# Optimization experiments

Measured on AMD Instinct MI355X. Metric: run time of the kernel, lower is better.

Reference implementation:

```python
import jax, jax.numpy as jnp
import numpy as np
import math

N_EMBED = 1024
N_HEAD = 16
BLOCK_SIZE = 2048

def setup_inputs() -> dict:
    key = jax.random.key(0)
    k1, k2, k3, k4, k5 = jax.random.split(key, 5)
    s = 0.02
    x = jax.random.normal(k1, (2, 2048, N_EMBED), dtype=jnp.float32)
    W_qkv = jax.random.normal(k2, (N_EMBED, 3 * N_EMBED), dtype=jnp.float32) * s
    b_qkv = jax.random.normal(k3, (3 * N_EMBED,), dtype=jnp.float32) * s
    W_out = jax.random.normal(k4, (N_EMBED, N_EMBED), dtype=jnp.float32) * s
    b_out = jax.random.normal(k5, (N_EMBED,), dtype=jnp.float32) * s
    return {"x": x, "W_qkv": W_qkv, "b_qkv": b_qkv, "W_out": W_out, "b_out": b_out}

def reference(x, W_qkv, b_qkv, W_out, b_out):
    b, s, d = x.shape
    hd = d // N_HEAD  # head dim
    qkv = x @ W_qkv + b_qkv                       # [b, s, 3d]
    q, k, v = jnp.split(qkv, 3, axis=-1)
    # [b, h, s, hd]
    q = q.reshape(b, s, N_HEAD, hd).transpose(0, 2, 1, 3)
    k = k.reshape(b, s, N_HEAD, hd).transpose(0, 2, 1, 3)
    v = v.reshape(b, s, N_HEAD, hd).transpose(0, 2, 1, 3)
    scale = 1.0 / math.sqrt(hd)
    sims = jnp.einsum('bhqd,bhkd->bhqk', q, k) * scale  # [b, h, s, s]
    causal = jnp.tril(jnp.ones((s, s), dtype=bool))
    sims = jnp.where(causal[None, None], sims, -jnp.inf)
    probs = jax.nn.softmax(sims, axis=-1)
    attn = jnp.einsum('bhqk,bhkd->bhqd', probs, v)       # [b, h, s, hd]
    attn = attn.transpose(0, 2, 1, 3).reshape(b, s, d)
    return attn @ W_out + b_out
```

## Files before the change

### kernel.cpp

```cpp
#include <hip/hip_runtime.h>
#include <hip/hip_bf16.h>

typedef __attribute__((ext_vector_type(8))) short short8;
typedef __attribute__((ext_vector_type(4))) short short4v;
typedef __attribute__((ext_vector_type(4))) float f32x4;
typedef __attribute__((ext_vector_type(16))) float f32x16;
typedef __attribute__((ext_vector_type(4))) unsigned int u32x4;
typedef unsigned short u16;

__device__ __forceinline__ u16 f2bf(float f) {
  __hip_bfloat16 h = __float2bfloat16(f);
  return __builtin_bit_cast(unsigned short, h);
}

__device__ __forceinline__ unsigned pack2(float lo, float hi) {
  return (unsigned)f2bf(lo) | ((unsigned)f2bf(hi) << 16);
}

__device__ __forceinline__ void gload16(const u16* g, u16* l) {
  __builtin_amdgcn_global_load_lds(
      (const __attribute__((address_space(1))) unsigned int*)g,
      (__attribute__((address_space(3))) unsigned int*)l, 16, 0, 0);
}

__global__ void prep_kernel(const float* __restrict__ x,
                            const float* __restrict__ Wqkv,
                            const float* __restrict__ Wout,
                            u16* __restrict__ Xb,
                            u16* __restrict__ WqkvT,
                            u16* __restrict__ WoutT) {
  __shared__ float tile[32][33];
  const int b = blockIdx.x, tid = threadIdx.x;
  if (b < 4096) {
    const int i = (b * 256 + tid) * 4;
    float4 f = *(const float4*)(x + i);
    uint2 pk;
    pk.x = pack2(f.x, f.y);
    pk.y = pack2(f.z, f.w);
    *(uint2*)(Xb + i) = pk;
    return;
  }
  const float* in;
  u16* out;
  int N, bx, by;
  if (b < 7168) {
    in = Wqkv; out = WqkvT; N = 3072;
    const int bb = b - 4096;
    bx = bb % 96; by = bb / 96;
  } else {
    in = Wout; out = WoutT; N = 1024;
    const int bb = b - 7168;
    bx = bb % 32; by = bb / 32;
  }
  const int n0 = bx * 32, k0 = by * 32;
  const int tx = tid & 31, ty = tid >> 5;
#pragma unroll
  for (int r = 0; r < 4; ++r) {
    const int k = ty + r * 8;
    tile[k][tx] = in[(size_t)(k0 + k) * N + n0 + tx];
  }
  __syncthreads();
#pragma unroll
  for (int r = 0; r < 4; ++r) {
    const int n = ty + r * 8;
    out[(size_t)(n0 + n) * 1024 + k0 + tx] = f2bf(tile[tx][n]);
  }
}

template <int EPI, int BN, int WPE>
__global__ __launch_bounds__(256, WPE) void gemm_kernel(const u16* __restrict__ A,
                                                        const u16* __restrict__ Bt,
                                                        const float* __restrict__ bias,
                                                        void* __restrict__ outp) {
  __shared__ u16 Al[128 * 64];
  __shared__ u16 Bl[BN * 64];
  constexpr int NF = BN / 32;
  const int tid = threadIdx.x;
  const int lane = tid & 63, wid = tid >> 6;
  const int l15 = lane & 15, lg = lane >> 4;
  const int wm = wid >> 1, wn = wid & 1;
  const int m0 = blockIdx.y * 128, n0 = blockIdx.x * BN;

  f32x4 acc[4][NF] = {};

  for (int k0 = 0; k0 < 1024; k0 += 64) {
    __syncthreads();
#pragma unroll
    for (int i = 0; i < 4; ++i) {
      const int p = i * 4096 + tid * 16;
      const int row = p >> 7;
      const int lslot = ((p >> 4) & 7) ^ (row & 7);
      gload16(A + (size_t)(m0 + row) * 1024 + k0 + lslot * 8, Al + i * 2048 + wid * 512);
    }
#pragma unroll
    for (int i = 0; i < NF; ++i) {
      const int p = i * 4096 + tid * 16;
      const int row = p >> 7;
      const int lslot = ((p >> 4) & 7) ^ (row & 7);
      gload16(Bt + (size_t)(n0 + row) * 1024 + k0 + lslot * 8, Bl + i * 2048 + wid * 512);
    }
    __syncthreads();
#pragma unroll
    for (int ks = 0; ks < 2; ++ks) {
      short8 af[4], bfr[NF];
#pragma unroll
      for (int m = 0; m < 4; ++m) {
        const int row = wm * 64 + m * 16 + l15;
        af[m] = *(const short8*)((const char*)Al + row * 128 + (((ks * 4 + lg) ^ (row & 7)) << 4));
      }
#pragma unroll
      for (int n = 0; n < NF; ++n) {
        const int row = wn * (BN / 2) + n * 16 + l15;
        bfr[n] = *(const short8*)((const char*)Bl + row * 128 + (((ks * 4 + lg) ^ (row & 7)) << 4));
      }
#pragma unroll
      for (int m = 0; m < 4; ++m)
#pragma unroll
        for (int n = 0; n < NF; ++n)
          acc[m][n] = __builtin_amdgcn_mfma_f32_16x16x32_bf16(af[m], bfr[n], acc[m][n], 0, 0, 0);
    }
  }

  if (EPI == 0) {
    u16* qkv = (u16*)outp;
#pragma unroll
    for (int m = 0; m < 4; ++m)
#pragma unroll
      for (int n = 0; n < NF; ++n) {
        const int gcol = n0 + wn * (BN / 2) + n * 16 + l15;
        const int which = gcol >> 10, dd = gcol & 1023;
        const int h = dd >> 6, hd = dd & 63;
        const float bb = bias[gcol];
        const int grow0 = m0 + wm * 64 + m * 16 + lg * 4;
        const int b = grow0 >> 11, s0 = grow0 & 2047;
        if (which == 2) {
          const int bsub = (s0 >> 2) & 3;
          const int bper = (bsub == 1) ? 2 : (bsub == 2) ? 1 : bsub;
          const int s0p = (s0 & ~15) | (bper << 2);
          short4v pk;
#pragma unroll
          for (int j = 0; j < 4; ++j) pk[j] = (short)f2bf(acc[m][n][j] + bb);
          *(short4v*)(qkv + (size_t)2 * 4194304 + ((size_t)(b * 16 + h) * 64 + hd) * 2048 + s0p) = pk;
        } else {
          const float sc = (which == 0) ? 0.18033688011112042f : 1.0f;
#pragma unroll
          for (int j = 0; j < 4; ++j) {
            float v = (acc[m][n][j] + bb) * sc;
            qkv[(size_t)which * 4194304 + ((size_t)(b * 16 + h) * 2048 + s0 + j) * 64 + hd] = f2bf(v);
          }
        }
      }
  } else {
    float* O = (float*)outp;
#pragma unroll
    for (int m = 0; m < 4; ++m)
#pragma unroll
      for (int n = 0; n < NF; ++n) {
        const int gcol = n0 + wn * (BN / 2) + n * 16 + l15;
        const float bb = bias[gcol];
#pragma unroll
        for (int j = 0; j < 4; ++j) {
          const int grow = m0 + wm * 64 + m * 16 + lg * 4 + j;
          O[(size_t)grow * 1024 + gcol] = acc[m][n][j] + bb;
        }
      }
  }
}

__global__ __launch_bounds__(512, 4) void attn_kernel(const u16* __restrict__ Q,
                                                      const u16* __restrict__ K,
                                                      const u16* __restrict__ VT,
                                                      u16* __restrict__ Aout) {
  const int d = blockIdx.x;
  const int xcd = d & 7, slot = d >> 3;
  const int bh = xcd + 8 * (slot >> 4);
  const int p = slot & 15;
  const int tid = threadIdx.x, lane = tid & 63, wid = tid >> 6;
  const int l31 = lane & 31, h = lane >> 5;
  const int tl = wid >> 2, qs = (wid >> 1) & 1, kp = wid & 1;

  __shared__ __align__(16) char smem[36864];
  u16(*Kl)[4096] = (u16(*)[4096])smem;
  u16(*Vl)[4096] = (u16(*)[4096])(smem + 16384);

  const u16* Qb = Q + (size_t)bh * 2048 * 64;
  const u16* Kb = K + (size_t)bh * 2048 * 64;
  const u16* Vb = VT + (size_t)bh * 64 * 2048;

  const int tile = tl ? p : (31 - p);
  const int q0 = tile * 64 + qs * 32;
  const int R = 32 - p;

  short8 qf[4];
#pragma unroll
  for (int ks = 0; ks < 4; ++ks)
    qf[ks] = *(const short8*)(Qb + (size_t)(q0 + l31) * 64 + ks * 16 + h * 8);

  short8 ones;
#pragma unroll
  for (int j = 0; j < 8; ++j) ones[j] = (short)0x3F80;

  f32x16 acc[2] = {};
  f32x16 acc_l = {};

  const int srow = tid >> 3;
  const int ssc = ((tid & 7) ^ (srow & 7)) * 8;
  auto stage = [&](int buf, size_t kb) {
    gload16(Kb + (kb + srow) * 64 + ssc, &Kl[buf][wid * 512]);
    gload16(Vb + (size_t)srow * 2048 + kb + ssc, &Vl[buf][wid * 512]);
  };

  stage(0, 0);
  __syncthreads();

  for (int t = 0; t < R; ++t) {
    const int cur = t & 1;
    if (t + 1 < R) stage(cur ^ 1, (size_t)(t + 1) * 64);

    const int kvbase = t * 64 + kp * 32;
    if (kvbase <= q0 + 31) {
      short8 kf[4], vf[2][2];
      const int krow = kp * 32 + l31;
#pragma unroll
      for (int ks = 0; ks < 4; ++ks)
        kf[ks] = *(const short8*)((const char*)&Kl[cur][0] + krow * 128 +
                                  (((ks * 2 + h) ^ (krow & 7)) << 4));
#pragma unroll
      for (int n = 0; n < 2; ++n)
#pragma unroll
        for (int ks = 0; ks < 2; ++ks) {
          const int row = n * 32 + l31;
          vf[n][ks] = *(const short8*)((const char*)&Vl[cur][0] + row * 128 +
                                       (((kp * 4 + ks * 2 + h) ^ (row & 7)) << 4));
        }

      f32x16 sa = {};
      __builtin_amdgcn_s_setprio(1);
#pragma unroll
      for (int ks = 0; ks < 4; ++ks)
        sa = __builtin_amdgcn_mfma_f32_32x32x16_bf16(kf[ks], qf[ks], sa, 0, 0, 0);
      __builtin_amdgcn_s_setprio(0);

      if (kvbase == q0) {
#pragma unroll
        for (int r = 0; r < 16; ++r) {
          const int kvr = (r & 3) + 8 * (r >> 2) + 4 * h;
          if (kvr > l31) sa[r] = -1e30f;
        }
      }
#pragma unroll
      for (int r = 0; r < 16; ++r) sa[r] = exp2f(sa[r]);
      unsigned c[8];
#pragma unroll
      for (int i = 0; i < 8; ++i) c[i] = pack2(sa[2 * i], sa[2 * i + 1]);
      const short8 pk0 = __builtin_bit_cast(short8, (u32x4){c[0], c[1], c[2], c[3]});
      const short8 pk1 = __builtin_bit_cast(short8, (u32x4){c[4], c[5], c[6], c[7]});
      __builtin_amdgcn_s_setprio(1);
      acc_l = __builtin_amdgcn_mfma_f32_32x32x16_bf16(ones, pk0, acc_l, 0, 0, 0);
      acc_l = __builtin_amdgcn_mfma_f32_32x32x16_bf16(ones, pk1, acc_l, 0, 0, 0);
#pragma unroll
      for (int n = 0; n < 2; ++n) {
        acc[n] = __builtin_amdgcn_mfma_f32_32x32x16_bf16(vf[n][0], pk0, acc[n], 0, 0, 0);
        acc[n] = __builtin_amdgcn_mfma_f32_32x32x16_bf16(vf[n][1], pk1, acc[n], 0, 0, 0);
      }
      __builtin_amdgcn_s_setprio(0);
    }
    __syncthreads();
  }

  float* pp = (float*)smem + (((tl << 1) | qs) * 64 + lane) * 36;
  if (kp == 1) {
    pp[0] = acc_l[0];
#pragma unroll
    for (int n = 0; n < 2; ++n)
#pragma unroll
      for (int r = 0; r < 16; ++r) pp[2 + n * 16 + r] = acc[n][r];
  }
  __syncthreads();
  if (kp == 0) {
    const int b = bh >> 4, hh = bh & 15;
    const float inv = 1.0f / (acc_l[0] + pp[0]);
    u16* rowp = Aout + (size_t)(b * 2048 + q0 + l31) * 1024 + hh * 64;
#pragma unroll
    for (int n = 0; n < 2; ++n)
#pragma unroll
      for (int r = 0; r < 16; r += 2) {
        const int hd = n * 32 + (r & 3) + 8 * (r >> 2) + 4 * h;
        const float v0 = (acc[n][r] + pp[2 + n * 16 + r]) * inv;
        const float v1 = (acc[n][r + 1] + pp[2 + n * 16 + r + 1]) * inv;
        *(unsigned*)(rowp + hd) = pack2(v0, v1);
      }
  }
}

extern "C" void kernel_launch(void* const* d_in, const int* in_sizes, int n_in,
                              void* d_out, int out_size, void* d_ws, size_t ws_size,
                              hipStream_t stream) {
  const float* x = (const float*)d_in[0];
  const float* Wqkv = (const float*)d_in[1];
  const float* bqkv = (const float*)d_in[2];
  const float* Wout = (const float*)d_in[3];
  const float* bout = (const float*)d_in[4];

  char* ws = (char*)d_ws;
  u16* Xb = (u16*)(ws + 0);
  u16* WqkvT = (u16*)(ws + 8388608);
  u16* WoutT = (u16*)(ws + 14680064);
  u16* QKV = (u16*)(ws + 16777216);
  u16* Attn = Xb;

  prep_kernel<<<8192, 256, 0, stream>>>(x, Wqkv, Wout, Xb, WqkvT, WoutT);
  gemm_kernel<0, 128, 3><<<dim3(24, 32), 256, 0, stream>>>(Xb, WqkvT, bqkv, QKV);
  attn_kernel<<<512, 512, 0, stream>>>(QKV, QKV + 4194304, QKV + 8388608, Attn);
  gemm_kernel<1, 64, 2><<<dim3(16, 32), 256, 0, stream>>>(Attn, WoutT, bout, d_out);
}
```

Baseline: 97.75 us.

## Fuse x fp32-to-bf16 conversion into QKV GEMM load; retile output GEMM

The separate conversion pass that turned x into bf16 in the prep kernel is removed. The QKV GEMM now reads fp32 x straight from global memory, packs it to bf16 in registers, and stores it into swizzled LDS. This saves a full write and re-read of the bf16 activation copy and shrinks the prep launch. The output projection GEMM moves to 64x64 tiles with more blocks and higher occupancy. The cost is that the QKV GEMM now issues synchronous fp32 loads with twice the bytes instead of async global-to-LDS copies, and these are re-read for each of the 24 column blocks.

```diff
diff --git a/kernel.cpp b/kernel.cpp
--- a/kernel.cpp
+++ b/kernel.cpp
@@ -23,33 +23,21 @@
       (__attribute__((address_space(3))) unsigned int*)l, 16, 0, 0);
 }
 
-__global__ void prep_kernel(const float* __restrict__ x,
-                            const float* __restrict__ Wqkv,
+__global__ void prep_kernel(const float* __restrict__ Wqkv,
                             const float* __restrict__ Wout,
-                            u16* __restrict__ Xb,
                             u16* __restrict__ WqkvT,
                             u16* __restrict__ WoutT) {
   __shared__ float tile[32][33];
   const int b = blockIdx.x, tid = threadIdx.x;
-  if (b < 4096) {
-    const int i = (b * 256 + tid) * 4;
-    float4 f = *(const float4*)(x + i);
-    uint2 pk;
-    pk.x = pack2(f.x, f.y);
-    pk.y = pack2(f.z, f.w);
-    *(uint2*)(Xb + i) = pk;
-    return;
-  }
   const float* in;
   u16* out;
   int N, bx, by;
-  if (b < 7168) {
+  if (b < 3072) {
     in = Wqkv; out = WqkvT; N = 3072;
-    const int bb = b - 4096;
-    bx = bb % 96; by = bb / 96;
+    bx = b % 96; by = b / 96;
   } else {
     in = Wout; out = WoutT; N = 1024;
-    const int bb = b - 7168;
+    const int bb = b - 3072;
     bx = bb % 32; by = bb / 32;
   }
   const int n0 = bx * 32, k0 = by * 32;
@@ -67,45 +55,62 @@
   }
 }
 
-template <int EPI, int BN, int WPE>
-__global__ __launch_bounds__(256, WPE) void gemm_kernel(const u16* __restrict__ A,
+template <int EPI, int BM, int BN, int WPE>
+__global__ __launch_bounds__(256, WPE) void gemm_kernel(const void* __restrict__ Ap,
                                                         const u16* __restrict__ Bt,
                                                         const float* __restrict__ bias,
                                                         void* __restrict__ outp) {
-  __shared__ u16 Al[128 * 64];
+  constexpr int MF = BM / 32;
+  constexpr int NF = BN / 32;
+  __shared__ u16 Al[BM * 64];
   __shared__ u16 Bl[BN * 64];
-  constexpr int NF = BN / 32;
   const int tid = threadIdx.x;
   const int lane = tid & 63, wid = tid >> 6;
   const int l15 = lane & 15, lg = lane >> 4;
   const int wm = wid >> 1, wn = wid & 1;
-  const int m0 = blockIdx.y * 128, n0 = blockIdx.x * BN;
-
-  f32x4 acc[4][NF] = {};
+  const int m0 = blockIdx.y * BM, n0 = blockIdx.x * BN;
+
+  f32x4 acc[MF][NF] = {};
 
   for (int k0 = 0; k0 < 1024; k0 += 64) {
     __syncthreads();
 #pragma unroll
-    for (int i = 0; i < 4; ++i) {
-      const int p = i * 4096 + tid * 16;
-      const int row = p >> 7;
-      const int lslot = ((p >> 4) & 7) ^ (row & 7);
-      gload16(A + (size_t)(m0 + row) * 1024 + k0 + lslot * 8, Al + i * 2048 + wid * 512);
-    }
-#pragma unroll
     for (int i = 0; i < NF; ++i) {
-      const int p = i * 4096 + tid * 16;
-      const int row = p >> 7;
-      const int lslot = ((p >> 4) & 7) ^ (row & 7);
+      const int row = i * 32 + (tid >> 3);
+      const int lslot = (tid & 7) ^ (row & 7);
       gload16(Bt + (size_t)(n0 + row) * 1024 + k0 + lslot * 8, Bl + i * 2048 + wid * 512);
     }
+    if (EPI == 0) {
+      const float* X = (const float*)Ap;
+#pragma unroll
+      for (int i = 0; i < MF; ++i) {
+        const int row = i * 32 + (tid >> 3);
+        const int slot = tid & 7;
+        const int lslot = slot ^ (row & 7);
+        const float* src = X + (size_t)(m0 + row) * 1024 + k0 + lslot * 8;
+        const float4 a = *(const float4*)src;
+        const float4 b = *(const float4*)(src + 4);
+        u32x4 w;
+        w[0] = pack2(a.x, a.y); w[1] = pack2(a.z, a.w);
+        w[2] = pack2(b.x, b.y); w[3] = pack2(b.z, b.w);
+        *(u32x4*)(Al + row * 64 + slot * 8) = w;
+      }
+    } else {
+      const u16* A = (const u16*)Ap;
+#pragma unroll
+      for (int i = 0; i < MF; ++i) {
+        const int row = i * 32 + (tid >> 3);
+        const int lslot = (tid & 7) ^ (row & 7);
+        gload16(A + (size_t)(m0 + row) * 1024 + k0 + lslot * 8, Al + i * 2048 + wid * 512);
+      }
+    }
     __syncthreads();
 #pragma unroll
     for (int ks = 0; ks < 2; ++ks) {
-      short8 af[4], bfr[NF];
-#pragma unroll
-      for (int m = 0; m < 4; ++m) {
-        const int row = wm * 64 + m * 16 + l15;
+      short8 af[MF], bfr[NF];
+#pragma unroll
+      for (int m = 0; m < MF; ++m) {
+        const int row = wm * (BM / 2) + m * 16 + l15;
         af[m] = *(const short8*)((const char*)Al + row * 128 + (((ks * 4 + lg) ^ (row & 7)) << 4));
       }
 #pragma unroll
@@ -114,7 +119,7 @@
         bfr[n] = *(const short8*)((const char*)Bl + row * 128 + (((ks * 4 + lg) ^ (row & 7)) << 4));
       }
 #pragma unroll
-      for (int m = 0; m < 4; ++m)
+      for (int m = 0; m < MF; ++m)
 #pragma unroll
         for (int n = 0; n < NF; ++n)
           acc[m][n] = __builtin_amdgcn_mfma_f32_16x16x32_bf16(af[m], bfr[n], acc[m][n], 0, 0, 0);
@@ -124,14 +129,14 @@
   if (EPI == 0) {
     u16* qkv = (u16*)outp;
 #pragma unroll
-    for (int m = 0; m < 4; ++m)
+    for (int m = 0; m < MF; ++m)
 #pragma unroll
       for (int n = 0; n < NF; ++n) {
         const int gcol = n0 + wn * (BN / 2) + n * 16 + l15;
         const int which = gcol >> 10, dd = gcol & 1023;
         const int h = dd >> 6, hd = dd & 63;
         const float bb = bias[gcol];
-        const int grow0 = m0 + wm * 64 + m * 16 + lg * 4;
+        const int grow0 = m0 + wm * (BM / 2) + m * 16 + lg * 4;
         const int b = grow0 >> 11, s0 = grow0 & 2047;
         if (which == 2) {
           const int bsub = (s0 >> 2) & 3;
@@ -153,14 +158,14 @@
   } else {
     float* O = (float*)outp;
 #pragma unroll
-    for (int m = 0; m < 4; ++m)
+    for (int m = 0; m < MF; ++m)
 #pragma unroll
       for (int n = 0; n < NF; ++n) {
         const int gcol = n0 + wn * (BN / 2) + n * 16 + l15;
         const float bb = bias[gcol];
 #pragma unroll
         for (int j = 0; j < 4; ++j) {
-          const int grow = m0 + wm * 64 + m * 16 + lg * 4 + j;
+          const int grow = m0 + wm * (BM / 2) + m * 16 + lg * 4 + j;
           O[(size_t)grow * 1024 + gcol] = acc[m][n][j] + bb;
         }
       }
@@ -303,14 +308,13 @@
   const float* bout = (const float*)d_in[4];
 
   char* ws = (char*)d_ws;
-  u16* Xb = (u16*)(ws + 0);
+  u16* Attn = (u16*)(ws + 0);
   u16* WqkvT = (u16*)(ws + 8388608);
   u16* WoutT = (u16*)(ws + 14680064);
   u16* QKV = (u16*)(ws + 16777216);
-  u16* Attn = Xb;
-
-  prep_kernel<<<8192, 256, 0, stream>>>(x, Wqkv, Wout, Xb, WqkvT, WoutT);
-  gemm_kernel<0, 128, 3><<<dim3(24, 32), 256, 0, stream>>>(Xb, WqkvT, bqkv, QKV);
+
+  prep_kernel<<<4096, 256, 0, stream>>>(Wqkv, Wout, WqkvT, WoutT);
+  gemm_kernel<0, 128, 128, 3><<<dim3(24, 32), 256, 0, stream>>>(x, WqkvT, bqkv, QKV);
   attn_kernel<<<512, 512, 0, stream>>>(QKV, QKV + 4194304, QKV + 8388608, Attn);
-  gemm_kernel<1, 64, 2><<<dim3(16, 32), 256, 0, stream>>>(Attn, WoutT, bout, d_out);
-}
+  gemm_kernel<1, 64, 64, 4><<<dim3(16, 64), 256, 0, stream>>>(Attn, WoutT, bout, d_out);
+}
```

New measurement: 104.9 us. +7.3%, slower.
